# Optimization experiments

Measured on AMD Instinct MI355X. Metric: run time of the kernel, lower is better.

## Reference

```python
import jax, jax.numpy as jnp
import numpy as np

H = 16       # num_attention_heads
HKV = 4      # num_key_value_heads
HD = 128     # head_dim
G = H // HKV # num_key_value_groups


def setup_inputs() -> dict:
    key = jax.random.key(0)
    ks = jax.random.split(key, 7)
    s = 0.02
    B, S, D = 2, 2048, 2048
    return {
        "hidden_states": jax.random.normal(ks[0], (B, S, D), jnp.float32),
        "Wq": jax.random.normal(ks[1], (D, H * HD), jnp.float32) * s,
        "Wk": jax.random.normal(ks[2], (D, HKV * HD), jnp.float32) * s,
        "Wv": jax.random.normal(ks[3], (D, HKV * HD), jnp.float32) * s,
        "Wg": jax.random.normal(ks[4], (H * HD, HKV), jnp.float32) * s,
        "Wd": jax.random.normal(ks[5], (HKV * HD, HKV), jnp.float32) * s,
        "Wo": jax.random.normal(ks[6], (H * HD, D), jnp.float32) * s,
    }


def reference(hidden_states, Wq, Wk, Wv, Wg, Wd, Wo):
    b, s, _ = hidden_states.shape
    scale = HD ** -0.5

    q_flat = hidden_states @ Wq                    # [b,s,H*HD]
    k_flat = hidden_states @ Wk                    # [b,s,HKV*HD]
    v_flat = hidden_states @ Wv                    # [b,s,HKV*HD]

    gate = q_flat @ Wg                             # [b,s,HKV] (per query pos)
    delta = v_flat @ Wd                            # [b,s,HKV] (per key pos)
    # attn_bias: [b,HKV,key_len] after transpose; broadcast over query dim
    bias = (jax.nn.sigmoid(gate) * delta).transpose(0, 2, 1)  # [b,HKV,s]

    # [b,HKV,G,s,HD] query grouped by kv-head; [b,HKV,s,HD] key/value
    q = q_flat.reshape(b, s, HKV, G, HD).transpose(0, 2, 3, 1, 4)
    k = k_flat.reshape(b, s, HKV, HD).transpose(0, 2, 1, 3)
    v = v_flat.reshape(b, s, HKV, HD).transpose(0, 2, 1, 3)

    scores = jnp.einsum('bngqd,bnkd->bngqk', q, k) * scale  # [b,HKV,G,s,s]
    logits = scores + bias[:, :, None, None, :]

    causal = jnp.tril(jnp.ones((s, s), dtype=bool))
    # 'relu' mask: key positions allowed only where relu(bias) > 0
    allowed = causal[None, None, None] & (bias > 0)[:, :, None, None, :]
    neg = jnp.finfo(logits.dtype).min
    logits = jnp.where(allowed, logits, neg)

    p = jax.nn.softmax(logits, axis=-1)
    o = jnp.einsum('bngqk,bnkd->bngqd', p, v)               # [b,HKV,G,s,HD]
    o = o.transpose(0, 3, 1, 2, 4).reshape(b, s, H * HD)
    return o @ Wo
```

## Files before the change

### kernel.cpp

```cpp
#include <hip/hip_runtime.h>
#include <hip/hip_bf16.h>
#include <cmath>
#include <cstdint>

typedef __attribute__((ext_vector_type(8))) short short8;
typedef __attribute__((ext_vector_type(4))) float floatx4;
typedef __attribute__((ext_vector_type(4))) unsigned int uintx4;

typedef const __attribute__((address_space(1))) unsigned int* gas_p;
typedef __attribute__((address_space(3))) unsigned int* las_p;

#define LOG2E 1.4426950408889634f

__device__ inline unsigned short f2bf(float f) {
  unsigned int u = __builtin_bit_cast(unsigned int, f);
  unsigned int r = (u + 0x7FFFu + ((u >> 16) & 1u)) >> 16;
  return (unsigned short)r;
}
__device__ inline float bf2f(unsigned short h) {
  unsigned int u = ((unsigned int)h) << 16;
  return __builtin_bit_cast(float, u);
}

__global__ void k_f32_to_bf16(const float* __restrict__ in, unsigned short* __restrict__ out, int n4) {
  int i = blockIdx.x * 256 + threadIdx.x;
  if (i >= n4) return;
  float4 v = reinterpret_cast<const float4*>(in)[i];
  uint2 o;
  o.x = (unsigned)f2bf(v.x) | ((unsigned)f2bf(v.y) << 16);
  o.y = (unsigned)f2bf(v.z) | ((unsigned)f2bf(v.w) << 16);
  reinterpret_cast<uint2*>(out)[i] = o;
}

__global__ void k_transpose_w(const float* __restrict__ in, unsigned short* __restrict__ out,
                              int K, int N, float scl) {
  __shared__ float t[32][33];
  int n0 = blockIdx.x * 32, k0 = blockIdx.y * 32;
  int tx = threadIdx.x & 31, ty = threadIdx.x >> 5;
  #pragma unroll
  for (int r = ty; r < 32; r += 8)
    t[r][tx] = in[(long)(k0 + r) * N + n0 + tx];
  __syncthreads();
  #pragma unroll
  for (int r = ty; r < 32; r += 8)
    out[(long)(n0 + r) * K + k0 + tx] = f2bf(t[tx][r] * scl);
}

__global__ void k_wproj(const float* __restrict__ W, const float* __restrict__ Ws,
                        float* __restrict__ out, int Kw) {
  int d = blockIdx.x;
  float a0 = 0, a1 = 0, a2 = 0, a3 = 0;
  for (int j = threadIdx.x; j < Kw; j += 256) {
    float w = W[(long)d * Kw + j];
    float4 g = reinterpret_cast<const float4*>(Ws)[j];
    a0 += w * g.x; a1 += w * g.y; a2 += w * g.z; a3 += w * g.w;
  }
  #pragma unroll
  for (int off = 1; off < 64; off <<= 1) {
    a0 += __shfl_xor(a0, off, 64); a1 += __shfl_xor(a1, off, 64);
    a2 += __shfl_xor(a2, off, 64); a3 += __shfl_xor(a3, off, 64);
  }
  __shared__ float red[4][4];
  if ((threadIdx.x & 63) == 0) {
    int wv = threadIdx.x >> 6;
    red[wv][0] = a0; red[wv][1] = a1; red[wv][2] = a2; red[wv][3] = a3;
  }
  __syncthreads();
  if (threadIdx.x < 4) {
    int nn = threadIdx.x;
    out[d * 4 + nn] = red[0][nn] + red[1][nn] + red[2][nn] + red[3][nn];
  }
}

__global__ void k_bias(const float* __restrict__ hs, const float* __restrict__ Wqg,
                       const float* __restrict__ Wvd, float* __restrict__ bias) {
  int row = blockIdx.x;
  int b = row >> 11, s = row & 2047;
  float g0 = 0, g1 = 0, g2 = 0, g3 = 0, d0 = 0, d1 = 0, d2 = 0, d3 = 0;
  const float* h = hs + (long)row * 2048;
  for (int j = threadIdx.x; j < 2048; j += 256) {
    float x = h[j];
    float4 a = reinterpret_cast<const float4*>(Wqg)[j];
    float4 c = reinterpret_cast<const float4*>(Wvd)[j];
    g0 += x * a.x; g1 += x * a.y; g2 += x * a.z; g3 += x * a.w;
    d0 += x * c.x; d1 += x * c.y; d2 += x * c.z; d3 += x * c.w;
  }
  #pragma unroll
  for (int off = 1; off < 64; off <<= 1) {
    g0 += __shfl_xor(g0, off, 64); g1 += __shfl_xor(g1, off, 64);
    g2 += __shfl_xor(g2, off, 64); g3 += __shfl_xor(g3, off, 64);
    d0 += __shfl_xor(d0, off, 64); d1 += __shfl_xor(d1, off, 64);
    d2 += __shfl_xor(d2, off, 64); d3 += __shfl_xor(d3, off, 64);
  }
  __shared__ float red[4][8];
  if ((threadIdx.x & 63) == 0) {
    int wv = threadIdx.x >> 6;
    red[wv][0] = g0; red[wv][1] = g1; red[wv][2] = g2; red[wv][3] = g3;
    red[wv][4] = d0; red[wv][5] = d1; red[wv][6] = d2; red[wv][7] = d3;
  }
  __syncthreads();
  if (threadIdx.x < 4) {
    int nn = threadIdx.x;
    float gg = red[0][nn] + red[1][nn] + red[2][nn] + red[3][nn];
    float dd = red[0][4 + nn] + red[1][4 + nn] + red[2][4 + nn] + red[3][4 + nn];
    float sig = 1.0f / (1.0f + __expf(-gg));
    float v = sig * dd;
    bias[(b * 4 + nn) * 2048 + s] = (v > 0.0f) ? v * LOG2E : -INFINITY;
  }
}

template <int WRITE_BF16>
__global__ __launch_bounds__(256, 2) void k_gemm_bt(
    const unsigned short* __restrict__ A, const unsigned short* __restrict__ Bt,
    void* __restrict__ Cout, int M, int N, int K) {
  __shared__ __align__(16) unsigned short As[128 * 32];
  __shared__ __align__(16) unsigned short Bs[128 * 32];
  const int tid = threadIdx.x;
  const int lane = tid & 63, wave = tid >> 6;
  const int quad = lane >> 4, l16 = lane & 15;
  const long bm = (long)blockIdx.y * 128, bn = (long)blockIdx.x * 128;
  const int wm = (wave >> 1) * 64, wn = (wave & 1) * 64;

  const floatx4 fz = {0.f, 0.f, 0.f, 0.f};
  floatx4 acc[4][4];
  #pragma unroll
  for (int i = 0; i < 4; i++)
    #pragma unroll
    for (int j = 0; j < 4; j++) acc[i][j] = fz;

  const int r0 = tid >> 2, c0 = (tid & 3) * 8;
  const unsigned short* Ag = A + (bm + r0) * K + c0;
  const unsigned short* Bg = Bt + (bn + r0) * K + c0;
  unsigned short* AsW0 = As + (wave * 16) * 32;
  unsigned short* AsW1 = As + (wave * 16 + 64) * 32;
  unsigned short* BsW0 = Bs + (wave * 16) * 32;
  unsigned short* BsW1 = Bs + (wave * 16 + 64) * 32;

  for (int kt = 0; kt < K; kt += 32) {
    __syncthreads();
    __builtin_amdgcn_global_load_lds((gas_p)(const void*)(Ag + kt),
                                     (las_p)(void*)AsW0, 16, 0, 0);
    __builtin_amdgcn_global_load_lds((gas_p)(const void*)(Ag + (long)64 * K + kt),
                                     (las_p)(void*)AsW1, 16, 0, 0);
    __builtin_amdgcn_global_load_lds((gas_p)(const void*)(Bg + kt),
                                     (las_p)(void*)BsW0, 16, 0, 0);
    __builtin_amdgcn_global_load_lds((gas_p)(const void*)(Bg + (long)64 * K + kt),
                                     (las_p)(void*)BsW1, 16, 0, 0);
    __syncthreads();
    short8 af[4], bf[4];
    #pragma unroll
    for (int i = 0; i < 4; i++)
      af[i] = *reinterpret_cast<const short8*>(&As[(wm + i * 16 + l16) * 32 + quad * 8]);
    #pragma unroll
    for (int j = 0; j < 4; j++)
      bf[j] = *reinterpret_cast<const short8*>(&Bs[(wn + j * 16 + l16) * 32 + quad * 8]);
    #pragma unroll
    for (int i = 0; i < 4; i++)
      #pragma unroll
      for (int j = 0; j < 4; j++)
        acc[i][j] = __builtin_amdgcn_mfma_f32_16x16x32_bf16(af[i], bf[j], acc[i][j], 0, 0, 0);
  }
  #pragma unroll
  for (int i = 0; i < 4; i++)
    #pragma unroll
    for (int j = 0; j < 4; j++)
      #pragma unroll
      for (int r = 0; r < 4; r++) {
        const long row = bm + wm + i * 16 + quad * 4 + r;
        const long col = bn + wn + j * 16 + l16;
        const float v = acc[i][j][r];
        if (WRITE_BF16)
          ((unsigned short*)Cout)[row * N + col] = f2bf(v);
        else
          ((float*)Cout)[row * N + col] = v;
      }
}

__global__ void k_transpose_v(const unsigned short* __restrict__ qkv, unsigned short* __restrict__ vt) {
  __shared__ unsigned short t[32][33];
  int c0 = blockIdx.x * 32, s0 = blockIdx.y * 32, b = blockIdx.z;
  int tx = threadIdx.x & 31, ty = threadIdx.x >> 5;
  #pragma unroll
  for (int r = ty; r < 32; r += 8)
    t[r][tx] = qkv[((long)(b * 2048 + s0 + r)) * 3072 + 2560 + c0 + tx];
  __syncthreads();
  #pragma unroll
  for (int r = ty; r < 32; r += 8)
    vt[((long)(b * 512 + c0 + r)) * 2048 + s0 + tx] = t[tx][r];
}

__global__ void k_vmean2(const unsigned short* __restrict__ vT, float* __restrict__ vmean) {
  const int row = blockIdx.x;
  const int tid = threadIdx.x, lane = tid & 63, wave = tid >> 6;
  uintx4 v = reinterpret_cast<const uintx4*>(vT + (long)row * 2048)[tid];
  float s = 0.f;
  #pragma unroll
  for (int i = 0; i < 4; i++) {
    unsigned u = v[i];
    s += bf2f((unsigned short)(u & 0xffff)) + bf2f((unsigned short)(u >> 16));
  }
  #pragma unroll
  for (int off = 1; off < 64; off <<= 1) s += __shfl_xor(s, off, 64);
  __shared__ float red[4];
  if (lane == 0) red[wave] = s;
  __syncthreads();
  if (tid == 0) vmean[row] = (red[0] + red[1] + red[2] + red[3]) * (1.0f / 2048.0f);
}

__global__ __launch_bounds__(256, 3) void k_attn(
    const unsigned short* __restrict__ qkv,
    const float* __restrict__ biasb,
    const unsigned short* __restrict__ vT,
    const float* __restrict__ vmean,
    unsigned short* __restrict__ o)
{
  int idx = blockIdx.x;
  const int g = idx & 3;
  const int n = (idx >> 2) & 3;
  const int b = (idx >> 4) & 1;
  const int qt = 31 - (idx >> 5);
  const int tid = threadIdx.x, lane = tid & 63, wave = tid >> 6;
  const int quad = lane >> 4, l16 = lane & 15;
  const int q0 = qt * 64 + wave * 16;

  __shared__ __align__(16) unsigned short Ks[64 * 144];
  __shared__ __align__(16) unsigned short Vs[128 * 72];
  __shared__ __align__(16) unsigned short Ps[4 * 16 * 72];
  unsigned short* Psw = Ps + wave * 1152;

  short8 qf[4];
  {
    const unsigned short* qp = qkv + (long)(b * 2048) * 3072 + (n * 4 + g) * 128;
    #pragma unroll
    for (int ks = 0; ks < 4; ks++)
      qf[ks] = *reinterpret_cast<const short8*>(
          qp + (long)(q0 + l16) * 3072 + ks * 32 + quad * 8);
  }

  const floatx4 fz = {0.f, 0.f, 0.f, 0.f};
  floatx4 oacc[8];
  #pragma unroll
  for (int j = 0; j < 8; j++) oacc[j] = fz;
  float mrow = -INFINITY, lrow = 0.0f;

  const float* biasrow = biasb + (b * 4 + n) * 2048;
  const unsigned short* kbase = qkv + (long)(b * 2048) * 3072 + 2048 + n * 128;
  const unsigned short* vbase = vT + (long)(b * 512 + n * 128) * 2048;
  const int kk_ = tid >> 4, hdo_ = (tid & 15) * 8;
  const int hd_ = tid >> 3, ko_ = (tid & 7) * 8;

  uintx4 kreg[4], vreg[4];
  float4 breg[4];
  {
    const unsigned short* kp = kbase;
    const unsigned short* vp = vbase;
    #pragma unroll
    for (int it = 0; it < 4; it++)
      kreg[it] = *reinterpret_cast<const uintx4*>(kp + (long)(kk_ + it * 16) * 3072 + hdo_);
    #pragma unroll
    for (int it = 0; it < 4; it++)
      vreg[it] = *reinterpret_cast<const uintx4*>(vp + (long)(hd_ + it * 32) * 2048 + ko_);
    #pragma unroll
    for (int kt = 0; kt < 4; kt++)
      breg[kt] = *reinterpret_cast<const float4*>(biasrow + kt * 16 + quad * 4);
  }

  const int kend = qt * 64 + 64;
  for (int k0 = 0; k0 < kend; k0 += 64) {
    __syncthreads();
    #pragma unroll
    for (int it = 0; it < 4; it++)
      *reinterpret_cast<uintx4*>(&Ks[(kk_ + it * 16) * 144 + hdo_]) = kreg[it];
    #pragma unroll
    for (int it = 0; it < 4; it++)
      *reinterpret_cast<uintx4*>(&Vs[(hd_ + it * 32) * 72 + ko_]) = vreg[it];
    float4 bcur[4];
    #pragma unroll
    for (int kt = 0; kt < 4; kt++) bcur[kt] = breg[kt];

    if (k0 + 64 < kend) {
      const unsigned short* kp = kbase + (long)(k0 + 64) * 3072;
      const unsigned short* vp = vbase + (k0 + 64);
      #pragma unroll
      for (int it = 0; it < 4; it++)
        kreg[it] = *reinterpret_cast<const uintx4*>(kp + (long)(kk_ + it * 16) * 3072 + hdo_);
      #pragma unroll
      for (int it = 0; it < 4; it++)
        vreg[it] = *reinterpret_cast<const uintx4*>(vp + (long)(hd_ + it * 32) * 2048 + ko_);
      #pragma unroll
      for (int kt = 0; kt < 4; kt++)
        breg[kt] = *reinterpret_cast<const float4*>(biasrow + (k0 + 64) + kt * 16 + quad * 4);
    }
    __syncthreads();

    const bool active = (k0 <= q0 + 15);
    if (active) {
      floatx4 sacc[4];
      #pragma unroll
      for (int kt = 0; kt < 4; kt++)
        sacc[kt] = (floatx4){bcur[kt].x, bcur[kt].y, bcur[kt].z, bcur[kt].w};
      __builtin_amdgcn_s_setprio(1);
      #pragma unroll
      for (int ks = 0; ks < 4; ks++) {
        short8 kf[4];
        #pragma unroll
        for (int kt = 0; kt < 4; kt++)
          kf[kt] = *reinterpret_cast<const short8*>(&Ks[(kt * 16 + l16) * 144 + ks * 32 + quad * 8]);
        #pragma unroll
        for (int kt = 0; kt < 4; kt++)
          sacc[kt] = __builtin_amdgcn_mfma_f32_16x16x32_bf16(kf[kt], qf[ks], sacc[kt], 0, 0, 0);
      }
      __builtin_amdgcn_s_setprio(0);

      const bool full = (k0 + 63 <= q0);
      if (!full) {
        const int diff = (q0 + l16) - (k0 + quad * 4);
        #pragma unroll
        for (int kt = 0; kt < 4; kt++)
          #pragma unroll
          for (int r = 0; r < 4; r++)
            if (kt * 16 + r > diff) sacc[kt][r] = -INFINITY;
      }
      float mx = -INFINITY;
      #pragma unroll
      for (int kt = 0; kt < 4; kt++)
        #pragma unroll
        for (int r = 0; r < 4; r++) mx = fmaxf(mx, sacc[kt][r]);
      mx = fmaxf(mx, __shfl_xor(mx, 16, 64));
      mx = fmaxf(mx, __shfl_xor(mx, 32, 64));
      const float mn = fmaxf(mrow, mx);
      const float mnc = fmaxf(mn, -1e38f);
      const float alpha = __builtin_amdgcn_exp2f(mrow - mnc);
      float rs = 0.0f;
      unsigned pk[4][2];
      #pragma unroll
      for (int kt = 0; kt < 4; kt++) {
        #pragma unroll
        for (int r = 0; r < 4; r++) {
          float p = __builtin_amdgcn_exp2f(sacc[kt][r] - mnc);
          sacc[kt][r] = p;
          rs += p;
        }
        #pragma unroll
        for (int r2 = 0; r2 < 2; r2++)
          pk[kt][r2] = (unsigned)f2bf(sacc[kt][2 * r2]) | ((unsigned)f2bf(sacc[kt][2 * r2 + 1]) << 16);
      }
      rs += __shfl_xor(rs, 16, 64);
      rs += __shfl_xor(rs, 32, 64);
      mrow = mn;
      lrow = lrow * alpha + rs;

      float al[4];
      #pragma unroll
      for (int r = 0; r < 4; r++) al[r] = __shfl(alpha, quad * 4 + r, 64);
      #pragma unroll
      for (int j = 0; j < 8; j++)
        #pragma unroll
        for (int r = 0; r < 4; r++) oacc[j][r] *= al[r];

      unsigned* Pd = reinterpret_cast<unsigned*>(Psw);
      #pragma unroll
      for (int kt = 0; kt < 4; kt++)
        #pragma unroll
        for (int r2 = 0; r2 < 2; r2++)
          Pd[l16 * 36 + kt * 8 + quad * 2 + r2] = pk[kt][r2];

      __builtin_amdgcn_s_setprio(1);
      #pragma unroll
      for (int ks2 = 0; ks2 < 2; ks2++) {
        short8 pf = *reinterpret_cast<const short8*>(&Psw[l16 * 72 + ks2 * 32 + quad * 8]);
        #pragma unroll
        for (int j = 0; j < 8; j++) {
          short8 vf = *reinterpret_cast<const short8*>(&Vs[(j * 16 + l16) * 72 + ks2 * 32 + quad * 8]);
          oacc[j] = __builtin_amdgcn_mfma_f32_16x16x32_bf16(pf, vf, oacc[j], 0, 0, 0);
        }
      }
      __builtin_amdgcn_s_setprio(0);
    }
  }

  const long obase = (long)(b * 2048) * 2048 + (n * 4 + g) * 128;
  #pragma unroll
  for (int r = 0; r < 4; r++) {
    const int qrow = q0 + quad * 4 + r;
    const float l = __shfl(lrow, quad * 4 + r, 64);
    const float inv = (l > 0.0f) ? 1.0f / l : 0.0f;
    #pragma unroll
    for (int j = 0; j < 8; j++) {
      const int hd = j * 16 + l16;
      float v = oacc[j][r] * inv;
      if (l <= 0.0f) v = vmean[(b * 4 + n) * 128 + hd];
      o[obase + (long)qrow * 2048 + hd] = f2bf(v);
    }
  }
}

extern "C" void kernel_launch(void* const* d_in, const int* in_sizes, int n_in,
                              void* d_out, int out_size, void* d_ws, size_t ws_size,
                              hipStream_t stream) {
  const float* hs = (const float*)d_in[0];
  const float* Wq = (const float*)d_in[1];
  const float* Wk = (const float*)d_in[2];
  const float* Wv = (const float*)d_in[3];
  const float* Wg = (const float*)d_in[4];
  const float* Wd = (const float*)d_in[5];
  const float* Wo = (const float*)d_in[6];
  float* out = (float*)d_out;

  char* ws = (char*)d_ws;
  unsigned short* hsb   = (unsigned short*)(ws);
  unsigned short* Wcomb = (unsigned short*)(ws + 16777216);
  unsigned short* Wot   = (unsigned short*)(ws + 29360128);
  float*  Wqg   = (float*)(ws + 37748736);
  float*  Wvd   = (float*)(ws + 37781504);
  float*  biasb = (float*)(ws + 37814272);
  unsigned short* qkv = (unsigned short*)(ws + 37879808);
  unsigned short* vT  = (unsigned short*)(ws + 63045632);
  float*  vmean = (float*)(ws + 67239936);
  unsigned short* ob  = (unsigned short*)(ws + 67244032);

  const float QSCALE = 0.08838834764831845f * LOG2E;

  k_f32_to_bf16<<<2097152 / 256, 256, 0, stream>>>(hs, hsb, 2097152);

  {
    dim3 g1(2048 / 32, 2048 / 32);
    dim3 g2(512 / 32, 2048 / 32);
    k_transpose_w<<<g1, 256, 0, stream>>>(Wq, Wcomb, 2048, 2048, QSCALE);
    k_transpose_w<<<g2, 256, 0, stream>>>(Wk, Wcomb + (long)2048 * 2048, 2048, 512, 1.0f);
    k_transpose_w<<<g2, 256, 0, stream>>>(Wv, Wcomb + (long)2560 * 2048, 2048, 512, 1.0f);
    k_transpose_w<<<g1, 256, 0, stream>>>(Wo, Wot, 2048, 2048, 1.0f);
  }

  k_wproj<<<2048, 256, 0, stream>>>(Wq, Wg, Wqg, 2048);
  k_wproj<<<2048, 256, 0, stream>>>(Wv, Wd, Wvd, 512);

  k_bias<<<4096, 256, 0, stream>>>(hs, Wqg, Wvd, biasb);

  {
    dim3 gq(3072 / 128, 4096 / 128);
    k_gemm_bt<1><<<gq, 256, 0, stream>>>(hsb, Wcomb, qkv, 4096, 3072, 2048);
  }

  {
    dim3 gv(16, 64, 2);
    k_transpose_v<<<gv, 256, 0, stream>>>(qkv, vT);
  }

  k_vmean2<<<1024, 256, 0, stream>>>(vT, vmean);

  k_attn<<<1024, 256, 0, stream>>>(qkv, biasb, vT, vmean, ob);

  {
    dim3 go(2048 / 128, 4096 / 128);
    k_gemm_bt<0><<<go, 256, 0, stream>>>(ob, Wot, out, 4096, 2048, 2048);
  }
}
```

Measured before the change: 345.9 us.

## Compact allowed key positions per head and skip masked keys in attention

Adds a scan kernel that compacts key positions with positive bias into an index list, and gather kernels that build compacted K and transposed V buffers. The attention kernel then loops only over the compacted keys up to a per-query-tile bound, applying the causal mask through the stored original indices. Since roughly half the biases are non-positive, this aims to cut attention FLOPs and memory traffic about in half. In exchange it adds several small preprocessing kernels and reuses the hidden-states bf16 workspace region, which is safe only because that buffer is dead by that point.

```diff
diff --git a/kernel.cpp b/kernel.cpp
--- a/kernel.cpp
+++ b/kernel.cpp
@@ -109,6 +109,81 @@
   }
 }
 
+__global__ void k_scan(const float* __restrict__ biasb, int* __restrict__ idx,
+                       float* __restrict__ biasc, int* __restrict__ kendArr) {
+  const int bn = blockIdx.x;
+  const int t = threadIdx.x;
+  const float* br = biasb + bn * 2048;
+  float v[8]; int pred[8]; int c = 0;
+  #pragma unroll
+  for (int i = 0; i < 8; i++) {
+    v[i] = br[t * 8 + i];
+    pred[i] = (v[i] > -1e30f) ? 1 : 0;
+    c += pred[i];
+  }
+  __shared__ int cnts[256];
+  __shared__ int offs[257];
+  cnts[t] = c;
+  __syncthreads();
+  if (t == 0) {
+    int acc = 0;
+    for (int i = 0; i < 256; i++) { offs[i] = acc; acc += cnts[i]; }
+    offs[256] = acc;
+  }
+  __syncthreads();
+  int off = offs[t];
+  #pragma unroll
+  for (int i = 0; i < 8; i++) {
+    if (pred[i]) {
+      idx[bn * 2048 + off] = t * 8 + i;
+      biasc[bn * 2048 + off] = v[i];
+      off++;
+    }
+  }
+  const int cnt = offs[256];
+  for (int j = cnt + t; j < 2048; j += 256) {
+    idx[bn * 2048 + j] = 0x7FFFFFFF;
+    biasc[bn * 2048 + j] = -INFINITY;
+  }
+  if (t == 0) {
+    for (int qt = 0; qt < 32; qt++) {
+      int pc = offs[(qt + 1) * 8];
+      kendArr[bn * 32 + qt] = (pc + 63) & ~63;
+    }
+  }
+}
+
+__global__ void k_gatherk(const unsigned short* __restrict__ qkv, const int* __restrict__ idx,
+                          unsigned short* __restrict__ Kc) {
+  const int bn = blockIdx.y, b = bn >> 2, n = bn & 3;
+  const int j = blockIdx.x * 16 + (threadIdx.x >> 4);
+  const int seg = threadIdx.x & 15;
+  const int s = idx[bn * 2048 + j];
+  uintx4 val = {0u, 0u, 0u, 0u};
+  if (s < 2048)
+    val = *reinterpret_cast<const uintx4*>(qkv + ((long)(b * 2048 + s)) * 3072 + 2048 + n * 128 + seg * 8);
+  *reinterpret_cast<uintx4*>(Kc + ((long)bn * 2048 + j) * 128 + seg * 8) = val;
+}
+
+__global__ void k_gathervt(const unsigned short* __restrict__ qkv, const int* __restrict__ idx,
+                           unsigned short* __restrict__ vTc) {
+  __shared__ unsigned short t[32][33];
+  const int bn = blockIdx.z, b = bn >> 2, n = bn & 3;
+  const int c0 = blockIdx.x * 32, j0 = blockIdx.y * 32;
+  const int tx = threadIdx.x & 31, ty = threadIdx.x >> 5;
+  #pragma unroll
+  for (int r = ty; r < 32; r += 8) {
+    const int s = idx[bn * 2048 + j0 + r];
+    t[r][tx] = (s < 2048)
+        ? qkv[((long)(b * 2048 + s)) * 3072 + 2560 + n * 128 + c0 + tx]
+        : (unsigned short)0;
+  }
+  __syncthreads();
+  #pragma unroll
+  for (int r = ty; r < 32; r += 8)
+    vTc[((long)bn * 128 + c0 + r) * 2048 + j0 + tx] = t[tx][r];
+}
+
 template <int WRITE_BF16>
 __global__ __launch_bounds__(256, 2) void k_gemm_bt(
     const unsigned short* __restrict__ A, const unsigned short* __restrict__ Bt,
@@ -209,8 +284,11 @@
 
 __global__ __launch_bounds__(256, 3) void k_attn(
     const unsigned short* __restrict__ qkv,
-    const float* __restrict__ biasb,
-    const unsigned short* __restrict__ vT,
+    const unsigned short* __restrict__ Kc,
+    const float* __restrict__ biasc,
+    const unsigned short* __restrict__ vTc,
+    const int* __restrict__ idxArr,
+    const int* __restrict__ kendArr,
     const float* __restrict__ vmean,
     unsigned short* __restrict__ o)
 {
@@ -222,10 +300,12 @@
   const int tid = threadIdx.x, lane = tid & 63, wave = tid >> 6;
   const int quad = lane >> 4, l16 = lane & 15;
   const int q0 = qt * 64 + wave * 16;
+  const int bn = b * 4 + n;
 
   __shared__ __align__(16) unsigned short Ks[64 * 144];
   __shared__ __align__(16) unsigned short Vs[128 * 72];
   __shared__ __align__(16) unsigned short Ps[4 * 16 * 72];
+  __shared__ __align__(16) int Is[64];
   unsigned short* Psw = Ps + wave * 1152;
 
   short8 qf[4];
@@ -243,29 +323,30 @@
   for (int j = 0; j < 8; j++) oacc[j] = fz;
   float mrow = -INFINITY, lrow = 0.0f;
 
-  const float* biasrow = biasb + (b * 4 + n) * 2048;
-  const unsigned short* kbase = qkv + (long)(b * 2048) * 3072 + 2048 + n * 128;
-  const unsigned short* vbase = vT + (long)(b * 512 + n * 128) * 2048;
+  const float* biasrow = biasc + bn * 2048;
+  const unsigned short* kbase = Kc + (long)bn * 2048 * 128;
+  const unsigned short* vbase = vTc + (long)bn * 128 * 2048;
+  const int* idxp = idxArr + bn * 2048;
+  const int kend = kendArr[bn * 32 + qt];
   const int kk_ = tid >> 4, hdo_ = (tid & 15) * 8;
   const int hd_ = tid >> 3, ko_ = (tid & 7) * 8;
 
   uintx4 kreg[4], vreg[4];
   float4 breg[4];
-  {
-    const unsigned short* kp = kbase;
-    const unsigned short* vp = vbase;
+  int ireg;
+  {
     #pragma unroll
     for (int it = 0; it < 4; it++)
-      kreg[it] = *reinterpret_cast<const uintx4*>(kp + (long)(kk_ + it * 16) * 3072 + hdo_);
+      kreg[it] = *reinterpret_cast<const uintx4*>(kbase + (long)(kk_ + it * 16) * 128 + hdo_);
     #pragma unroll
     for (int it = 0; it < 4; it++)
-      vreg[it] = *reinterpret_cast<const uintx4*>(vp + (long)(hd_ + it * 32) * 2048 + ko_);
+      vreg[it] = *reinterpret_cast<const uintx4*>(vbase + (long)(hd_ + it * 32) * 2048 + ko_);
     #pragma unroll
     for (int kt = 0; kt < 4; kt++)
       breg[kt] = *reinterpret_cast<const float4*>(biasrow + kt * 16 + quad * 4);
-  }
-
-  const int kend = qt * 64 + 64;
+    ireg = idxp[tid & 63];
+  }
+
   for (int k0 = 0; k0 < kend; k0 += 64) {
     __syncthreads();
     #pragma unroll
@@ -274,26 +355,29 @@
     #pragma unroll
     for (int it = 0; it < 4; it++)
       *reinterpret_cast<uintx4*>(&Vs[(hd_ + it * 32) * 72 + ko_]) = vreg[it];
+    if (tid < 64) Is[tid] = ireg;
     float4 bcur[4];
     #pragma unroll
     for (int kt = 0; kt < 4; kt++) bcur[kt] = breg[kt];
 
     if (k0 + 64 < kend) {
-      const unsigned short* kp = kbase + (long)(k0 + 64) * 3072;
+      const unsigned short* kp = kbase + (long)(k0 + 64) * 128;
       const unsigned short* vp = vbase + (k0 + 64);
       #pragma unroll
       for (int it = 0; it < 4; it++)
-        kreg[it] = *reinterpret_cast<const uintx4*>(kp + (long)(kk_ + it * 16) * 3072 + hdo_);
+        kreg[it] = *reinterpret_cast<const uintx4*>(kp + (long)(kk_ + it * 16) * 128 + hdo_);
       #pragma unroll
       for (int it = 0; it < 4; it++)
         vreg[it] = *reinterpret_cast<const uintx4*>(vp + (long)(hd_ + it * 32) * 2048 + ko_);
       #pragma unroll
       for (int kt = 0; kt < 4; kt++)
         breg[kt] = *reinterpret_cast<const float4*>(biasrow + (k0 + 64) + kt * 16 + quad * 4);
+      ireg = idxp[k0 + 64 + (tid & 63)];
     }
     __syncthreads();
 
-    const bool active = (k0 <= q0 + 15);
+    const int ifirst = Is[0];
+    const bool active = (ifirst <= q0 + 15);
     if (active) {
       floatx4 sacc[4];
       #pragma unroll
@@ -312,14 +396,18 @@
       }
       __builtin_amdgcn_s_setprio(0);
 
-      const bool full = (k0 + 63 <= q0);
+      const int ilast = Is[63];
+      const bool full = (ilast <= q0);
       if (!full) {
-        const int diff = (q0 + l16) - (k0 + quad * 4);
-        #pragma unroll
-        for (int kt = 0; kt < 4; kt++)
-          #pragma unroll
-          for (int r = 0; r < 4; r++)
-            if (kt * 16 + r > diff) sacc[kt][r] = -INFINITY;
+        const int qme = q0 + l16;
+        #pragma unroll
+        for (int kt = 0; kt < 4; kt++) {
+          const int4 iq = *reinterpret_cast<const int4*>(&Is[kt * 16 + quad * 4]);
+          if (iq.x > qme) sacc[kt][0] = -INFINITY;
+          if (iq.y > qme) sacc[kt][1] = -INFINITY;
+          if (iq.z > qme) sacc[kt][2] = -INFINITY;
+          if (iq.w > qme) sacc[kt][3] = -INFINITY;
+        }
       }
       float mx = -INFINITY;
       #pragma unroll
@@ -418,6 +506,11 @@
   unsigned short* vT  = (unsigned short*)(ws + 63045632);
   float*  vmean = (float*)(ws + 67239936);
   unsigned short* ob  = (unsigned short*)(ws + 67244032);
+  unsigned short* Kc    = (unsigned short*)(ws);
+  unsigned short* vTc   = (unsigned short*)(ws + 4194304);
+  int*   idxArr  = (int*)(ws + 8388608);
+  float* biascB  = (float*)(ws + 8454144);
+  int*   kendArr = (int*)(ws + 8519680);
 
   const float QSCALE = 0.08838834764831845f * LOG2E;
 
@@ -446,10 +539,17 @@
     dim3 gv(16, 64, 2);
     k_transpose_v<<<gv, 256, 0, stream>>>(qkv, vT);
   }
-
   k_vmean2<<<1024, 256, 0, stream>>>(vT, vmean);
 
-  k_attn<<<1024, 256, 0, stream>>>(qkv, biasb, vT, vmean, ob);
+  k_scan<<<8, 256, 0, stream>>>(biasb, idxArr, biascB, kendArr);
+  {
+    dim3 gk(128, 8);
+    k_gatherk<<<gk, 256, 0, stream>>>(qkv, idxArr, Kc);
+    dim3 gvt(4, 64, 8);
+    k_gathervt<<<gvt, 256, 0, stream>>>(qkv, idxArr, vTc);
+  }
+
+  k_attn<<<1024, 256, 0, stream>>>(qkv, Kc, biascB, vTc, idxArr, kendArr, vmean, ob);
 
   {
     dim3 go(2048 / 128, 4096 / 128);
```

Measured after the change: 334.9 us. -3.2%, faster.
